# Kernel optimization log

Measured on AMD Instinct MI355X. Metric: run time of the kernel, lower is better.

Reference implementation:

```python
import jax, jax.numpy as jnp
import numpy as np

TEMPERATURE = 8.0
EPS = 1e-06
NEG = -1e10


def setup_inputs() -> dict:
    key = jax.random.key(0)
    kq, kk, kv = jax.random.split(key, 3)
    B, L, D = 16, 4096, 64
    q = jax.random.normal(kq, (B, L, D), dtype=jnp.float32)
    k = jax.random.normal(kk, (B, L, D), dtype=jnp.float32)
    v = jax.random.normal(kv, (B, L, D), dtype=jnp.float32)
    mask = jnp.zeros((B, L), dtype=bool)  # pad mask: True = padded query row
    return {"q": q, "k": k, "v": v, "mask": mask}


def reference(q, k, v, mask):
    # scores: [B, Lq, Lk]
    attn = jnp.einsum("bqd,bkd->bqk", q, k) / (TEMPERATURE + EPS)
    L = k.shape[1]
    # causal mask (True above diagonal) OR pad mask broadcast over key dim
    causal = jnp.triu(jnp.ones((L, L), dtype=bool), k=1)  # [Lq, Lk]
    mask_ = causal[None, :, :] | mask[:, :, None]
    attn = jnp.where(mask_, NEG, attn)
    attn = jax.nn.softmax(attn, axis=2)
    # dropout is identity at inference (reference omits it)
    output = jnp.einsum("bqk,bkd->bqd", attn, v)
    return (output, attn)
```

## Files before the change

kernel.cpp:

```cpp
#include <hip/hip_runtime.h>
#include <hip/hip_bf16.h>

#define BB 16
#define LL 4096
#define DD 64

typedef __attribute__((ext_vector_type(8))) short bf16x8;
typedef __attribute__((ext_vector_type(4))) float f32x4;

#define KST 72
#define VST 72
#define PST 72

__device__ __forceinline__ short f2bf(float f) {
    unsigned u = __builtin_bit_cast(unsigned, f);
    u += 0x7FFFu + ((u >> 16) & 1u);
    return (short)(u >> 16);
}

__global__ void __launch_bounds__(256)
attn_fused(const float* __restrict__ Q, const float* __restrict__ Km,
           const float* __restrict__ Vm, const unsigned char* __restrict__ Mask,
           float* __restrict__ Out, float* __restrict__ Attn)
{
    __shared__ short sK[64 * KST];
    __shared__ short sV[64 * VST];
    __shared__ short sP[4][16 * PST];
    __shared__ unsigned char sPad[64];
    __shared__ int sAny;

    const int tid  = threadIdx.x;
    const int wave = tid >> 6, lane = tid & 63;
    const int l15  = lane & 15, quad = lane >> 4;
    const int b = blockIdx.y, qt = blockIdx.x;
    const int q0 = qt << 6;

    if (tid < 64) sPad[tid] = (Mask[b * LL + q0 + tid] != 0) ? 1 : 0;
    __syncthreads();
    if (wave == 0) {
        unsigned long long bm = __ballot(sPad[lane] != 0);
        if (lane == 0) sAny = (bm != 0ull) ? 1 : 0;
    }
    __syncthreads();
    const int kbCount = sAny ? (LL >> 6) : (qt + 1);

    {
        const float4 z = make_float4(0.f, 0.f, 0.f, 0.f);
        const int cstart = kbCount << 6;
        for (int r = 0; r < 16; ++r) {
            const int rg = q0 + (wave << 4) + r;
            float* rp = Attn + ((size_t)(b * LL + rg) << 12);
            for (int c = cstart + (lane << 2); c < LL; c += 256)
                *(float4*)(rp + c) = z;
        }
    }

    bf16x8 aq[2];
    {
        const float* qp = Q + (((size_t)(b * LL + q0 + (wave << 4) + l15)) << 6) + (quad << 3);
        #pragma unroll
        for (int ks = 0; ks < 2; ++ks) {
            float4 f0 = *(const float4*)(qp + ks * 32);
            float4 f1 = *(const float4*)(qp + ks * 32 + 4);
            bf16x8 a;
            a[0] = f2bf(f0.x); a[1] = f2bf(f0.y); a[2] = f2bf(f0.z); a[3] = f2bf(f0.w);
            a[4] = f2bf(f1.x); a[5] = f2bf(f1.y); a[6] = f2bf(f1.z); a[7] = f2bf(f1.w);
            aq[ks] = a;
        }
    }

    const float scale = 1.0f / 8.000001f;

    int rowg[4]; int padr[4]; float* attnRow[4];
    #pragma unroll
    for (int r = 0; r < 4; ++r) {
        const int rl = (wave << 4) + quad * 4 + r;
        rowg[r] = q0 + rl;
        padr[r] = sPad[rl];
        attnRow[r] = Attn + ((size_t)(b * LL + rowg[r]) << 12);
    }

    float lsum[4] = {0.f, 0.f, 0.f, 0.f};
    for (int kb = 0; kb < kbCount; ++kb) {
        __syncthreads();
        {
            const float* kp = Km + (((size_t)(b * LL + (kb << 6))) << 6);
            #pragma unroll
            for (int i = 0; i < 4; ++i) {
                const int f4 = i * 256 + tid;
                const int row = f4 >> 4, d4 = f4 & 15;
                float4 x = *(const float4*)(kp + (row << 6) + (d4 << 2));
                short4 s; s.x = f2bf(x.x); s.y = f2bf(x.y); s.z = f2bf(x.z); s.w = f2bf(x.w);
                *(short4*)&sK[row * KST + (d4 << 2)] = s;
            }
        }
        __syncthreads();
        #pragma unroll
        for (int sub = 0; sub < 4; ++sub) {
            f32x4 acc = {0.f, 0.f, 0.f, 0.f};
            #pragma unroll
            for (int ks = 0; ks < 2; ++ks) {
                bf16x8 bk = *(bf16x8*)&sK[(sub * 16 + l15) * KST + ks * 32 + (quad << 3)];
                acc = __builtin_amdgcn_mfma_f32_16x16x32_bf16(aq[ks], bk, acc, 0, 0, 0);
            }
            const int colg = (kb << 6) + sub * 16 + l15;
            #pragma unroll
            for (int r = 0; r < 4; ++r) {
                float e = padr[r] ? 1.0f
                        : ((colg <= rowg[r]) ? __expf(acc[r] * scale) : 0.0f);
                lsum[r] += e;
            }
        }
    }
    #pragma unroll
    for (int r = 0; r < 4; ++r) {
        float v = lsum[r];
        v += __shfl_xor(v, 1); v += __shfl_xor(v, 2);
        v += __shfl_xor(v, 4); v += __shfl_xor(v, 8);
        lsum[r] = 1.0f / v;
    }

    f32x4 oacc[4];
    #pragma unroll
    for (int i = 0; i < 4; ++i) oacc[i] = (f32x4){0.f, 0.f, 0.f, 0.f};

    for (int kb = 0; kb < kbCount; ++kb) {
        __syncthreads();
        {
            const float* kp = Km + (((size_t)(b * LL + (kb << 6))) << 6);
            #pragma unroll
            for (int i = 0; i < 4; ++i) {
                const int f4 = i * 256 + tid;
                const int row = f4 >> 4, d4 = f4 & 15;
                float4 x = *(const float4*)(kp + (row << 6) + (d4 << 2));
                short4 s; s.x = f2bf(x.x); s.y = f2bf(x.y); s.z = f2bf(x.z); s.w = f2bf(x.w);
                *(short4*)&sK[row * KST + (d4 << 2)] = s;
            }
            const float* vp = Vm + (((size_t)(b * LL + (kb << 6))) << 6);
            #pragma unroll
            for (int i = 0; i < 2; ++i) {
                const int task = i * 256 + tid;
                const int kp2 = task & 31;
                const int vd  = task >> 5;
                const float* vr = vp + (kp2 << 7) + (vd << 2);
                float4 a0 = *(const float4*)(vr);
                float4 a1 = *(const float4*)(vr + 64);
                #pragma unroll
                for (int jj = 0; jj < 4; ++jj) {
                    const float x0 = (&a0.x)[jj], x1 = (&a1.x)[jj];
                    unsigned dw = (unsigned)(unsigned short)f2bf(x0)
                                | ((unsigned)(unsigned short)f2bf(x1) << 16);
                    *(unsigned*)&sV[(vd * 4 + jj) * VST + (kp2 << 1)] = dw;
                }
            }
        }
        __syncthreads();
        #pragma unroll
        for (int sub = 0; sub < 4; ++sub) {
            f32x4 acc = {0.f, 0.f, 0.f, 0.f};
            #pragma unroll
            for (int ks = 0; ks < 2; ++ks) {
                bf16x8 bk = *(bf16x8*)&sK[(sub * 16 + l15) * KST + ks * 32 + (quad << 3)];
                acc = __builtin_amdgcn_mfma_f32_16x16x32_bf16(aq[ks], bk, acc, 0, 0, 0);
            }
            const int col  = sub * 16 + l15;
            const int colg = (kb << 6) + col;
            #pragma unroll
            for (int r = 0; r < 4; ++r) {
                float e = padr[r] ? 1.0f
                        : ((colg <= rowg[r]) ? __expf(acc[r] * scale) : 0.0f);
                float p = e * lsum[r];
                attnRow[r][colg] = p;
                sP[wave][(quad * 4 + r) * PST + col] = f2bf(p);
            }
        }
        __syncthreads();
        #pragma unroll
        for (int ks = 0; ks < 2; ++ks) {
            bf16x8 ap = *(bf16x8*)&sP[wave][l15 * PST + ks * 32 + (quad << 3)];
            #pragma unroll
            for (int dsub = 0; dsub < 4; ++dsub) {
                bf16x8 bv = *(bf16x8*)&sV[(dsub * 16 + l15) * VST + ks * 32 + (quad << 3)];
                oacc[dsub] = __builtin_amdgcn_mfma_f32_16x16x32_bf16(ap, bv, oacc[dsub], 0, 0, 0);
            }
        }
    }

    #pragma unroll
    for (int dsub = 0; dsub < 4; ++dsub) {
        #pragma unroll
        for (int r = 0; r < 4; ++r) {
            Out[(((size_t)(b * LL + rowg[r])) << 6) + dsub * 16 + l15] = oacc[dsub][r];
        }
    }
}

extern "C" void kernel_launch(void* const* d_in, const int* in_sizes, int n_in,
                              void* d_out, int out_size, void* d_ws, size_t ws_size,
                              hipStream_t stream) {
    const float* Q = (const float*)d_in[0];
    const float* K = (const float*)d_in[1];
    const float* V = (const float*)d_in[2];
    const unsigned char* M = (const unsigned char*)d_in[3];
    float* Out  = (float*)d_out;
    float* Attn = (float*)d_out + (size_t)BB * LL * DD;
    dim3 grid(LL / 64, BB);
    attn_fused<<<grid, 256, 0, stream>>>(Q, K, V, M, Out, Attn);
}
```

Before: 1.449 ms.

## Precompute bf16 K and transposed V in a prep kernel, load fragments directly

```diff
diff --git a/kernel.cpp b/kernel.cpp
--- a/kernel.cpp
+++ b/kernel.cpp
@@ -8,8 +8,6 @@
 typedef __attribute__((ext_vector_type(8))) short bf16x8;
 typedef __attribute__((ext_vector_type(4))) float f32x4;
 
-#define KST 72
-#define VST 72
 #define PST 72
 
 __device__ __forceinline__ short f2bf(float f) {
@@ -19,12 +17,50 @@
 }
 
 __global__ void __launch_bounds__(256)
-attn_fused(const float* __restrict__ Q, const float* __restrict__ Km,
-           const float* __restrict__ Vm, const unsigned char* __restrict__ Mask,
+prep_kv(const float* __restrict__ Km, const float* __restrict__ Vm,
+        short* __restrict__ Kb, short* __restrict__ Vt)
+{
+    __shared__ short sVt[64 * PST];
+    const int tid = threadIdx.x;
+    const int kb = blockIdx.x, b = blockIdx.y;
+    const size_t tbase = ((size_t)(b * LL + (kb << 6))) << 6;
+
+    const float* kp = Km + tbase;
+    short* ko = Kb + tbase;
+    #pragma unroll
+    for (int i = 0; i < 4; ++i) {
+        const int e = (i * 256 + tid) << 2;
+        float4 x = *(const float4*)(kp + e);
+        short4 s; s.x = f2bf(x.x); s.y = f2bf(x.y); s.z = f2bf(x.z); s.w = f2bf(x.w);
+        *(short4*)(ko + e) = s;
+    }
+
+    const float* vp = Vm + tbase;
+    #pragma unroll
+    for (int i = 0; i < 4; ++i) {
+        const int task = i * 256 + tid;
+        const int l = task >> 4, d4 = task & 15;
+        float4 x = *(const float4*)(vp + (l << 6) + (d4 << 2));
+        sVt[(d4 * 4 + 0) * PST + l] = f2bf(x.x);
+        sVt[(d4 * 4 + 1) * PST + l] = f2bf(x.y);
+        sVt[(d4 * 4 + 2) * PST + l] = f2bf(x.z);
+        sVt[(d4 * 4 + 3) * PST + l] = f2bf(x.w);
+    }
+    __syncthreads();
+    #pragma unroll
+    for (int i = 0; i < 2; ++i) {
+        const int task = i * 256 + tid;
+        const int d = task >> 3, c = task & 7;
+        bf16x8 v = *(bf16x8*)&sVt[d * PST + (c << 3)];
+        *(bf16x8*)(Vt + (((size_t)(b * 64 + d)) << 12) + (kb << 6) + (c << 3)) = v;
+    }
+}
+
+__global__ void __launch_bounds__(256)
+attn_fused(const float* __restrict__ Q, const short* __restrict__ Kb,
+           const short* __restrict__ Vt, const unsigned char* __restrict__ Mask,
            float* __restrict__ Out, float* __restrict__ Attn)
 {
-    __shared__ short sK[64 * KST];
-    __shared__ short sV[64 * VST];
     __shared__ short sP[4][16 * PST];
     __shared__ unsigned char sPad[64];
     __shared__ int sAny;
@@ -32,7 +68,8 @@
     const int tid  = threadIdx.x;
     const int wave = tid >> 6, lane = tid & 63;
     const int l15  = lane & 15, quad = lane >> 4;
-    const int b = blockIdx.y, qt = blockIdx.x;
+    const int b = blockIdx.y;
+    const int qt = (int)gridDim.x - 1 - (int)blockIdx.x;
     const int q0 = qt << 6;
 
     if (tid < 64) sPad[tid] = (Mask[b * LL + q0 + tid] != 0) ? 1 : 0;
@@ -69,7 +106,7 @@
         }
     }
 
-    const float scale = 1.0f / 8.000001f;
+    const float SCL2 = 1.4426950408889634f / 8.000001f;
 
     int rowg[4]; int padr[4]; float* attnRow[4];
     #pragma unroll
@@ -80,34 +117,28 @@
         attnRow[r] = Attn + ((size_t)(b * LL + rowg[r]) << 12);
     }
 
+    const short* kb_base = Kb + (((size_t)b * LL) << 6) + (quad << 3);
+    const short* vt_base = Vt + (((size_t)b * 64) << 12) + (quad << 3);
+
     float lsum[4] = {0.f, 0.f, 0.f, 0.f};
     for (int kb = 0; kb < kbCount; ++kb) {
-        __syncthreads();
-        {
-            const float* kp = Km + (((size_t)(b * LL + (kb << 6))) << 6);
-            #pragma unroll
-            for (int i = 0; i < 4; ++i) {
-                const int f4 = i * 256 + tid;
-                const int row = f4 >> 4, d4 = f4 & 15;
-                float4 x = *(const float4*)(kp + (row << 6) + (d4 << 2));
-                short4 s; s.x = f2bf(x.x); s.y = f2bf(x.y); s.z = f2bf(x.z); s.w = f2bf(x.w);
-                *(short4*)&sK[row * KST + (d4 << 2)] = s;
-            }
-        }
-        __syncthreads();
+        const short* kp = kb_base + (kb << 12);
+        bf16x8 bk[4][2];
+        #pragma unroll
+        for (int sub = 0; sub < 4; ++sub) {
+            bk[sub][0] = *(const bf16x8*)(kp + ((sub * 16 + l15) << 6));
+            bk[sub][1] = *(const bf16x8*)(kp + ((sub * 16 + l15) << 6) + 32);
+        }
         #pragma unroll
         for (int sub = 0; sub < 4; ++sub) {
             f32x4 acc = {0.f, 0.f, 0.f, 0.f};
-            #pragma unroll
-            for (int ks = 0; ks < 2; ++ks) {
-                bf16x8 bk = *(bf16x8*)&sK[(sub * 16 + l15) * KST + ks * 32 + (quad << 3)];
-                acc = __builtin_amdgcn_mfma_f32_16x16x32_bf16(aq[ks], bk, acc, 0, 0, 0);
-            }
+            acc = __builtin_amdgcn_mfma_f32_16x16x32_bf16(aq[0], bk[sub][0], acc, 0, 0, 0);
+            acc = __builtin_amdgcn_mfma_f32_16x16x32_bf16(aq[1], bk[sub][1], acc, 0, 0, 0);
             const int colg = (kb << 6) + sub * 16 + l15;
             #pragma unroll
             for (int r = 0; r < 4; ++r) {
                 float e = padr[r] ? 1.0f
-                        : ((colg <= rowg[r]) ? __expf(acc[r] * scale) : 0.0f);
+                        : ((colg <= rowg[r]) ? __builtin_amdgcn_exp2f(acc[r] * SCL2) : 0.0f);
                 lsum[r] += e;
             }
         }
@@ -125,64 +156,50 @@
     for (int i = 0; i < 4; ++i) oacc[i] = (f32x4){0.f, 0.f, 0.f, 0.f};
 
     for (int kb = 0; kb < kbCount; ++kb) {
-        __syncthreads();
-        {
-            const float* kp = Km + (((size_t)(b * LL + (kb << 6))) << 6);
-            #pragma unroll
-            for (int i = 0; i < 4; ++i) {
-                const int f4 = i * 256 + tid;
-                const int row = f4 >> 4, d4 = f4 & 15;
-                float4 x = *(const float4*)(kp + (row << 6) + (d4 << 2));
-                short4 s; s.x = f2bf(x.x); s.y = f2bf(x.y); s.z = f2bf(x.z); s.w = f2bf(x.w);
-                *(short4*)&sK[row * KST + (d4 << 2)] = s;
-            }
-            const float* vp = Vm + (((size_t)(b * LL + (kb << 6))) << 6);
-            #pragma unroll
-            for (int i = 0; i < 2; ++i) {
-                const int task = i * 256 + tid;
-                const int kp2 = task & 31;
-                const int vd  = task >> 5;
-                const float* vr = vp + (kp2 << 7) + (vd << 2);
-                float4 a0 = *(const float4*)(vr);
-                float4 a1 = *(const float4*)(vr + 64);
-                #pragma unroll
-                for (int jj = 0; jj < 4; ++jj) {
-                    const float x0 = (&a0.x)[jj], x1 = (&a1.x)[jj];
-                    unsigned dw = (unsigned)(unsigned short)f2bf(x0)
-                                | ((unsigned)(unsigned short)f2bf(x1) << 16);
-                    *(unsigned*)&sV[(vd * 4 + jj) * VST + (kp2 << 1)] = dw;
-                }
-            }
-        }
-        __syncthreads();
+        const short* kp = kb_base + (kb << 12);
+        bf16x8 bk[4][2];
+        #pragma unroll
+        for (int sub = 0; sub < 4; ++sub) {
+            bk[sub][0] = *(const bf16x8*)(kp + ((sub * 16 + l15) << 6));
+            bk[sub][1] = *(const bf16x8*)(kp + ((sub * 16 + l15) << 6) + 32);
+        }
+        f32x4 s4[4];
         #pragma unroll
         for (int sub = 0; sub < 4; ++sub) {
             f32x4 acc = {0.f, 0.f, 0.f, 0.f};
-            #pragma unroll
-            for (int ks = 0; ks < 2; ++ks) {
-                bf16x8 bk = *(bf16x8*)&sK[(sub * 16 + l15) * KST + ks * 32 + (quad << 3)];
-                acc = __builtin_amdgcn_mfma_f32_16x16x32_bf16(aq[ks], bk, acc, 0, 0, 0);
-            }
+            acc = __builtin_amdgcn_mfma_f32_16x16x32_bf16(aq[0], bk[sub][0], acc, 0, 0, 0);
+            acc = __builtin_amdgcn_mfma_f32_16x16x32_bf16(aq[1], bk[sub][1], acc, 0, 0, 0);
+            s4[sub] = acc;
+        }
+
+        const short* vp = vt_base + (kb << 6);
+        bf16x8 bv[4][2];
+        #pragma unroll
+        for (int dsub = 0; dsub < 4; ++dsub) {
+            bv[dsub][0] = *(const bf16x8*)(vp + (((size_t)(dsub * 16 + l15)) << 12));
+            bv[dsub][1] = *(const bf16x8*)(vp + (((size_t)(dsub * 16 + l15)) << 12) + 32);
+        }
+
+        #pragma unroll
+        for (int sub = 0; sub < 4; ++sub) {
             const int col  = sub * 16 + l15;
             const int colg = (kb << 6) + col;
             #pragma unroll
             for (int r = 0; r < 4; ++r) {
                 float e = padr[r] ? 1.0f
-                        : ((colg <= rowg[r]) ? __expf(acc[r] * scale) : 0.0f);
+                        : ((colg <= rowg[r]) ? __builtin_amdgcn_exp2f(s4[sub][r] * SCL2) : 0.0f);
                 float p = e * lsum[r];
                 attnRow[r][colg] = p;
                 sP[wave][(quad * 4 + r) * PST + col] = f2bf(p);
             }
         }
-        __syncthreads();
+
         #pragma unroll
         for (int ks = 0; ks < 2; ++ks) {
             bf16x8 ap = *(bf16x8*)&sP[wave][l15 * PST + ks * 32 + (quad << 3)];
             #pragma unroll
-            for (int dsub = 0; dsub < 4; ++dsub) {
-                bf16x8 bv = *(bf16x8*)&sV[(dsub * 16 + l15) * VST + ks * 32 + (quad << 3)];
-                oacc[dsub] = __builtin_amdgcn_mfma_f32_16x16x32_bf16(ap, bv, oacc[dsub], 0, 0, 0);
-            }
+            for (int dsub = 0; dsub < 4; ++dsub)
+                oacc[dsub] = __builtin_amdgcn_mfma_f32_16x16x32_bf16(ap, bv[dsub][ks], oacc[dsub], 0, 0, 0);
         }
     }
 
@@ -204,6 +221,11 @@
     const unsigned char* M = (const unsigned char*)d_in[3];
     float* Out  = (float*)d_out;
     float* Attn = (float*)d_out + (size_t)BB * LL * DD;
+
+    short* Kbf = (short*)d_ws;
+    short* Vtr = Kbf + (size_t)BB * LL * DD;
+
     dim3 grid(LL / 64, BB);
-    attn_fused<<<grid, 256, 0, stream>>>(Q, K, V, M, Out, Attn);
-}
+    prep_kv<<<grid, 256, 0, stream>>>(K, V, Kbf, Vtr);
+    attn_fused<<<grid, 256, 0, stream>>>(Q, Kbf, Vtr, M, Out, Attn);
+}
```

After: 1.617 ms. +11.5%, slower.
